# Kernel optimization log

Measured on AMD Instinct MI355X. Metric: run time of the kernel, lower is better.

The kernel has to match this reference:

```python
import jax, jax.numpy as jnp
import numpy as np

H, HEADS, LAYERS = 512, 4, 3
HD = H // HEADS
FFN = 4 * H
B, S = 4, 2048
EPS = 1e-5
SCALE_BASE = 512.0
GAMMAS = (1.0 - np.exp(np.linspace(np.log(1.0 / 32.0), np.log(1.0 / 512.0), HEADS))).astype(np.float32)


def _xpos(x, downscale):
    # x: [B, heads, L, d]; standard XPOS rotary with per-dim decay scale
    L, d = x.shape[-2], x.shape[-1]
    half = d // 2
    s = (jnp.arange(half, dtype=jnp.float32) + 0.4 * d) / (1.4 * d)          # [half]
    pos = jnp.arange(L, dtype=jnp.float32)
    scale = s[None, :] ** (pos[:, None] / SCALE_BASE)                         # [L, half]
    inv_freq = 1.0 / (10000.0 ** (jnp.arange(half, dtype=jnp.float32) / half))
    ang = pos[:, None] * inv_freq[None, :]                                    # [L, half]
    if downscale:
        scale = 1.0 / scale
    sin_s = jnp.repeat(jnp.sin(ang) * scale, 2, axis=-1)                      # [L, d]
    cos_s = jnp.repeat(jnp.cos(ang) * scale, 2, axis=-1)
    x1, x2 = x[..., 0::2], x[..., 1::2]
    rot = jnp.stack([-x2, x1], axis=-1).reshape(x.shape)                      # rotate_every_two
    return x * cos_s + rot * sin_s


def _layernorm(x, w, b):
    m = x.mean(-1, keepdims=True)
    v = ((x - m) ** 2).mean(-1, keepdims=True)
    return (x - m) / jnp.sqrt(v + EPS) * w + b


def _decay_mask(L):
    n = jnp.arange(L)
    nm = n[:, None] - n[None, :]
    g = jnp.asarray(GAMMAS)                                                   # [heads]
    # D[h,n,m] = gamma_h^(n-m) for n>=m else 0
    return jnp.where((nm >= 0)[None], g[:, None, None] ** jnp.maximum(nm, 0)[None], 0.0)


def _msr(X, WQ, WK, WV, WG, WO, gnw, gnb, D):
    # X: [B,S,H]; WQ/WK/WV: [heads,H,HD]; D: [heads,S,S]
    Q = _xpos(jnp.einsum('bsh,nhd->bnsd', X, WQ), False)
    K = _xpos(jnp.einsum('bsh,nhd->bnsd', X, WK), True)
    V = jnp.einsum('bsh,nhd->bnsd', X, WV)
    A = jnp.einsum('bnsd,bntd->bnst', Q, K) * D[None]                          # decay-weighted retention
    Y = jnp.einsum('bnst,bntd->bnsd', A, V)                                    # [B,heads,S,HD]
    Y = jnp.transpose(Y, (0, 2, 1, 3))                                         # [B,S,heads,HD] (head-major concat)
    m = Y.mean(-1, keepdims=True)
    v = ((Y - m) ** 2).mean(-1, keepdims=True)
    Yn = ((Y - m) / jnp.sqrt(v + EPS)).reshape(X.shape[0], X.shape[1], H) * gnw + gnb  # GroupNorm(heads, H)
    G = X @ WG
    return (G * jax.nn.sigmoid(G) * Yn) @ WO                                   # swish gate + out proj


def setup_inputs() -> dict:
    key = jax.random.key(0)
    ks = jax.random.split(key, 10)
    rn = lambda k, shape, sc: jax.random.normal(k, shape, jnp.float32) * sc
    return {
        'X': rn(ks[0], (B, S, H), 1.0),
        'WQ': rn(ks[1], (LAYERS, HEADS, H, HD), 1.0 / H),
        'WK': rn(ks[2], (LAYERS, HEADS, H, HD), 1.0 / H),
        'WV': rn(ks[3], (LAYERS, HEADS, H, HD), 1.0 / H),
        'WG': rn(ks[4], (LAYERS, H, H), 1.0 / H),
        'WO': rn(ks[5], (LAYERS, H, H), 1.0 / H),
        'gn_w': jnp.ones((LAYERS, H), jnp.float32),
        'gn_b': jnp.zeros((LAYERS, H), jnp.float32),
        'ln1_w': jnp.ones((LAYERS, H), jnp.float32),
        'ln1_b': jnp.zeros((LAYERS, H), jnp.float32),
        'ln2_w': jnp.ones((LAYERS, H), jnp.float32),
        'ln2_b': jnp.zeros((LAYERS, H), jnp.float32),
        'ffn_w1': rn(ks[6], (LAYERS, H, FFN), (2.0 / (H + FFN)) ** 0.5),
        'ffn_b1': jnp.zeros((LAYERS, FFN), jnp.float32),
        'ffn_w2': rn(ks[7], (LAYERS, FFN, H), (2.0 / (H + FFN)) ** 0.5),
        'ffn_b2': jnp.zeros((LAYERS, H), jnp.float32),
    }


def reference(X, WQ, WK, WV, WG, WO, gn_w, gn_b, ln1_w, ln1_b, ln2_w, ln2_b, ffn_w1, ffn_b1, ffn_w2, ffn_b2):
    D = _decay_mask(X.shape[1])
    for l in range(LAYERS):
        Y = _msr(_layernorm(X, ln1_w[l], ln1_b[l]), WQ[l], WK[l], WV[l], WG[l], WO[l], gn_w[l], gn_b[l], D) + X
        Hn = _layernorm(Y, ln2_w[l], ln2_b[l])
        X = jax.nn.gelu(Hn @ ffn_w1[l] + ffn_b1[l], approximate=False) @ ffn_w2[l] + ffn_b2[l] + Y
    return X, jnp.einsum('bsh,bth->bst', X, X)
```

## Files before the change

### kernel.cpp

```cpp
#include <hip/hip_runtime.h>
#include <math.h>

#define HH 512
#define NHEADS 4
#define HD 128
#define HALF 64
#define FFND 2048
#define BB 4
#define SS 2048
#define NLAYERS 3
#define ROWS (BB*SS)
#define EPSF 1e-5f
#define QKVGW 2048

typedef float f32x4 __attribute__((ext_vector_type(4)));
typedef float f32x16 __attribute__((ext_vector_type(16)));
typedef __bf16 bf16x8 __attribute__((ext_vector_type(8)));
typedef unsigned u32x2 __attribute__((ext_vector_type(2)));

__device__ __forceinline__ unsigned short f2bf(float f) {
    union { float f; unsigned u; } v; v.f = f;
    unsigned r = (v.u + 0x7FFFu + ((v.u >> 16) & 1u)) >> 16;
    return (unsigned short)r;
}
__device__ __forceinline__ float bf2f(unsigned short h) {
    union { unsigned u; float f; } v; v.u = ((unsigned)h) << 16;
    return v.f;
}
__device__ __forceinline__ void gl16(const void* g, void* l) {
    __builtin_amdgcn_global_load_lds((const __attribute__((address_space(1))) void*)g,
                                     (__attribute__((address_space(3))) void*)l, 16, 0, 0);
}
__device__ __forceinline__ bf16x8 ld8(const void* p) { return *(const bf16x8*)p; }
__device__ __forceinline__ unsigned laddr(void* p) {
    return (unsigned)(size_t)(__attribute__((address_space(3))) char*)p;
}
__device__ __forceinline__ u32x2 tr8(unsigned a) {
    u32x2 r;
    asm volatile("ds_read_b64_tr_b16 %0, %1" : "=v"(r) : "v"(a));
    return r;
}

__global__ void k_tables(float* __restrict__ cq, float* __restrict__ sq,
                         float* __restrict__ ck, float* __restrict__ sk) {
    int i = threadIdx.x;
    int s = blockIdx.x;
    float si   = ((float)i + 0.4f * (float)HD) / (1.4f * (float)HD);
    float scale = powf(si, (float)s / 512.0f);
    float invf = powf(10000.0f, -((float)i) / (float)HALF);
    float ang  = (float)s * invf;
    float c = cosf(ang), sn = sinf(ang);
    int idx = s * HALF + i;
    cq[idx] = c * scale;   sq[idx] = sn * scale;
    float is = 1.0f / scale;
    ck[idx] = c * is;      sk[idx] = sn * is;
}

__global__ __launch_bounds__(256) void k_wt(const float* __restrict__ src, unsigned short* __restrict__ dst,
                                            int K, int N, int zn, size_t sL, size_t sZ) {
    __shared__ float T[32][33];
    int n0 = blockIdx.x * 32, k0 = blockIdx.y * 32;
    int z = blockIdx.z;
    src += (size_t)z * (size_t)K * N;
    dst += (size_t)(z / zn) * sL + (size_t)(z % zn) * sZ;
    int tx = threadIdx.x & 31, ty = threadIdx.x >> 5;
    #pragma unroll
    for (int i = 0; i < 4; ++i) {
        int r = ty + i * 8;
        T[r][tx] = src[(size_t)(k0 + r) * N + n0 + tx];
    }
    __syncthreads();
    #pragma unroll
    for (int i = 0; i < 4; ++i) {
        int r = ty + i * 8;
        dst[(size_t)(n0 + r) * K + k0 + tx] = f2bf(T[tx][r]);
    }
}

__global__ __launch_bounds__(256) void k_ln(const float* __restrict__ x, const float* __restrict__ w,
                                            const float* __restrict__ b, unsigned short* __restrict__ y) {
    int lane = threadIdx.x & 63;
    size_t row = (size_t)blockIdx.x * 4 + (threadIdx.x >> 6);
    const float4* xr = (const float4*)(x + row * HH);
    float4 v0 = xr[lane * 2];
    float4 v1 = xr[lane * 2 + 1];
    float s  = v0.x + v0.y + v0.z + v0.w + v1.x + v1.y + v1.z + v1.w;
    float ss = v0.x*v0.x + v0.y*v0.y + v0.z*v0.z + v0.w*v0.w
             + v1.x*v1.x + v1.y*v1.y + v1.z*v1.z + v1.w*v1.w;
    for (int off = 32; off > 0; off >>= 1) {
        s  += __shfl_xor(s, off);
        ss += __shfl_xor(ss, off);
    }
    float m   = s * (1.0f / HH);
    float var = ss * (1.0f / HH) - m * m;
    float inv = rsqrtf(var + EPSF);
    int h0 = lane * 8;
    float4 wa = *(const float4*)(w + h0);
    float4 wb = *(const float4*)(w + h0 + 4);
    float4 ba = *(const float4*)(b + h0);
    float4 bb2 = *(const float4*)(b + h0 + 4);
    uint4 pk;
    pk.x = f2bf((v0.x - m) * inv * wa.x + ba.x) | ((unsigned)f2bf((v0.y - m) * inv * wa.y + ba.y) << 16);
    pk.y = f2bf((v0.z - m) * inv * wa.z + ba.z) | ((unsigned)f2bf((v0.w - m) * inv * wa.w + ba.w) << 16);
    pk.z = f2bf((v1.x - m) * inv * wb.x + bb2.x) | ((unsigned)f2bf((v1.y - m) * inv * wb.y + bb2.y) << 16);
    pk.w = f2bf((v1.z - m) * inv * wb.z + bb2.z) | ((unsigned)f2bf((v1.w - m) * inv * wb.w + bb2.w) << 16);
    *(uint4*)(y + row * HH + h0) = pk;
}

__global__ __launch_bounds__(256) void k_xpos(unsigned short* __restrict__ QG,
    const float* __restrict__ cq, const float* __restrict__ sq,
    const float* __restrict__ ck, const float* __restrict__ sk) {
    int row = blockIdx.x, p = threadIdx.x;
    int s = row & (SS - 1), n = p >> 6, i = p & 63;
    int ti = s * HALF + i;
    size_t qo = (size_t)row * QKVGW + n * HD + i * 2;
    unsigned qv = *(unsigned*)(QG + qo);
    float x1 = bf2f(qv & 0xffff), x2 = bf2f(qv >> 16);
    float c = cq[ti], sn = sq[ti];
    *(unsigned*)(QG + qo) = (unsigned)f2bf(x1 * c - x2 * sn) | ((unsigned)f2bf(x2 * c + x1 * sn) << 16);
    size_t ko = qo + 512;
    unsigned kv = *(unsigned*)(QG + ko);
    x1 = bf2f(kv & 0xffff); x2 = bf2f(kv >> 16);
    c = ck[ti]; sn = sk[ti];
    *(unsigned*)(QG + ko) = (unsigned)f2bf(x1 * c - x2 * sn) | ((unsigned)f2bf(x2 * c + x1 * sn) << 16);
}

__global__ __launch_bounds__(256) void k_zero(float* __restrict__ Y) {
    int idx = blockIdx.x * 256 + threadIdx.x;
    int bb = idx / 196608;
    int rem = idx - bb * 196608;
    float4 zz = {0.f, 0.f, 0.f, 0.f};
    *(float4*)(Y + (size_t)bb * (SS * HH) + (size_t)512 * HH + (size_t)rem * 4) = zz;
}

__global__ __launch_bounds__(256, 2) void k_ret(
    const unsigned short* __restrict__ QG, float* __restrict__ Y) {
    __shared__ __align__(16) char sm[81920];
    const int tid = threadIdx.x;
    const int lane = tid & 63, wv = tid >> 6;
    const int l31 = lane & 31, g2 = lane >> 5;
    const int b4 = (lane >> 4) & 1;
    const int bx = blockIdx.x;
    int xs, c0 = 0;
    if (bx < 16)      { xs = 15 - (bx >> 2); c0 = bx & 3; }
    else if (bx < 28) { int i = bx - 16; xs = 11 - i / 3; c0 = i % 3; }
    else if (bx < 36) { int i = bx - 28; xs = 7 - (i >> 1); c0 = i & 1; }
    else              { xs = 39 - bx; }
    const int hn = blockIdx.y, b = blockIdx.z;
    const int s0 = xs * 128;
    const int nt = 2 * xs + 2;
    const int tstart = c0 * 8;
    const int tend = min(nt, tstart + 8);
    const double la = -3.4657359027997265, lb = -6.238324625039508;
    const float gamma = (float)(1.0 - exp(la + (lb - la) * ((double)hn / 3.0)));
    const float l2g = log2f(gamma);
    const size_t rowbase = (size_t)b * SS;
    const int qcol = hn * HD, kcol = 512 + hn * HD, vcol = 1024 + hn * HD;
    const char* Gp = (const char*)QG;

    const int srow = s0 + wv * 32 + l31;
    bf16x8 qf[8];
    #pragma unroll
    for (int kc = 0; kc < 8; ++kc)
        qf[kc] = ld8(QG + (rowbase + srow) * QKVGW + qcol + kc * 16 + g2 * 8);

    float gq[4], gj[4];
    #pragma unroll
    for (int q = 0; q < 4; ++q) { gq[q] = exp2f(-l2g * (8.0f * q)); gj[q] = exp2f(-l2g * (float)q); }
    const float gt32m = exp2f(-l2g * 32.0f);

    f32x16 accy[4];
    #pragma unroll
    for (int d = 0; d < 4; ++d)
        #pragma unroll
        for (int e = 0; e < 16; ++e) accy[d][e] = 0.0f;

    const int sloc = wv * 32 + l31;
    const int ssw = (sloc & 7) << 4;
    const int r15 = (l31 & 15) << 4;

    auto stage = [&](int t0, int buf) {
        #pragma unroll
        for (int c = 0; c < 4; ++c) {
            int chunk = wv * 4 + c;
            int r = chunk * 4 + (lane >> 4);
            int w = ((lane & 15) * 16) ^ ((r & 15) << 4);
            gl16(Gp + ((rowbase + t0 + r) * QKVGW + kcol) * 2 + w, sm + buf * 16384 + chunk * 1024);
        }
        #pragma unroll
        for (int c = 0; c < 4; ++c) {
            int chunk = wv * 4 + c;
            int slot = chunk * 64 + lane;
            int sub = slot >> 3, w8 = slot & 7;
            int db = sub >> 4, tb = sub & 15;
            int tl = tb * 4 + (w8 >> 1);
            int d  = db * 16 + (w8 & 1) * 8;
            gl16(Gp + ((rowbase + t0 + tl) * QKVGW + vcol + d) * 2, sm + 32768 + buf * 16384 + chunk * 1024);
        }
    };

    int cur = 0;
    stage(tstart * 64, 0);
    for (int t = tstart; t < tend; ++t) {
        const int t0 = t * 64;
        if (t + 1 < tend) {
            stage((t + 1) * 64, cur ^ 1);
            asm volatile("s_waitcnt vmcnt(8)" ::: "memory");
        } else {
            asm volatile("s_waitcnt vmcnt(0)" ::: "memory");
        }
        __builtin_amdgcn_sched_barrier(0);
        __builtin_amdgcn_s_barrier();
        __builtin_amdgcn_sched_barrier(0);
        {
            const char* kb = sm + cur * 16384;
            f32x16 pacc0, pacc1;
            #pragma unroll
            for (int e = 0; e < 16; ++e) { pacc0[e] = 0.0f; pacc1[e] = 0.0f; }
            #pragma unroll
            for (int kc = 0; kc < 8; ++kc) {
                bf16x8 k0 = ld8(kb + l31 * 256 + ((kc * 32 + g2 * 16) ^ r15));
                bf16x8 k1 = ld8(kb + (32 + l31) * 256 + ((kc * 32 + g2 * 16) ^ r15));
                pacc0 = __builtin_amdgcn_mfma_f32_32x32x16_bf16(k0, qf[kc], pacc0, 0, 0, 0);
                pacc1 = __builtin_amdgcn_mfma_f32_32x32x16_bf16(k1, qf[kc], pacc1, 0, 0, 0);
            }
            const float G0 = exp2f(l2g * (float)(srow - t0 - g2 * 4));
            #pragma unroll
            for (int tb2 = 0; tb2 < 2; ++tb2) {
                const float gb = tb2 ? gt32m : 1.0f;
                #pragma unroll
                for (int q = 0; q < 4; ++q) {
                    int tbase = t0 + tb2 * 32 + q * 8 + g2 * 4;
                    float base = G0 * gb * gq[q];
                    float p0 = (tb2 ? pacc1 : pacc0)[q * 4 + 0];
                    float p1 = (tb2 ? pacc1 : pacc0)[q * 4 + 1];
                    float p2 = (tb2 ? pacc1 : pacc0)[q * 4 + 2];
                    float p3 = (tb2 ? pacc1 : pacc0)[q * 4 + 3];
                    unsigned short u0 = f2bf((srow >= tbase + 0) ? p0 * base * gj[0] : 0.0f);
                    unsigned short u1 = f2bf((srow >= tbase + 1) ? p1 * base * gj[1] : 0.0f);
                    unsigned short u2 = f2bf((srow >= tbase + 2) ? p2 * base * gj[2] : 0.0f);
                    unsigned short u3 = f2bf((srow >= tbase + 3) ? p3 * base * gj[3] : 0.0f);
                    u32x2 pk2;
                    pk2.x = (unsigned)u0 | ((unsigned)u1 << 16);
                    pk2.y = (unsigned)u2 | ((unsigned)u3 << 16);
                    *(u32x2*)(sm + 65536 + ((sloc * 128 + tb2 * 64 + q * 16 + g2 * 8) ^ ssw)) = pk2;
                }
            }
            bf16x8 pf[4];
            #pragma unroll
            for (int tc = 0; tc < 4; ++tc)
                pf[tc] = ld8(sm + 65536 + ((sloc * 128 + tc * 32 + g2 * 16) ^ ssw));
            const unsigned vbase = laddr(sm + 32768 + cur * 16384) + b4 * 2048 + g2 * 256 + (lane & 15) * 2;
            #pragma unroll
            for (int dblk = 0; dblk < 4; ++dblk) {
                u32x2 va[4], vb[4];
                #pragma unroll
                for (int tc = 0; tc < 4; ++tc) {
                    unsigned a0 = vbase + dblk * 4096 + tc * 512;
                    va[tc] = tr8(a0);
                    vb[tc] = tr8(a0 + 128);
                }
                asm volatile("s_waitcnt lgkmcnt(0)" ::: "memory");
                __builtin_amdgcn_sched_barrier(0);
                #pragma unroll
                for (int tc = 0; tc < 4; ++tc) {
                    union { u32x2 u[2]; bf16x8 v; } cvt;
                    cvt.u[0] = va[tc]; cvt.u[1] = vb[tc];
                    accy[dblk] = __builtin_amdgcn_mfma_f32_32x32x16_bf16(pf[tc], cvt.v, accy[dblk], 0, 0, 0);
                }
            }
        }
        __builtin_amdgcn_sched_barrier(0);
        __builtin_amdgcn_s_barrier();
        __builtin_amdgcn_sched_barrier(0);
        cur ^= 1;
    }
    if (xs < 4) {
        #pragma unroll
        for (int dblk = 0; dblk < 4; ++dblk)
            #pragma unroll
            for (int rg = 0; rg < 16; ++rg) {
                int sl2 = s0 + wv * 32 + (rg & 3) + (rg >> 2) * 8 + g2 * 4;
                Y[(rowbase + sl2) * HH + hn * HD + dblk * 32 + l31] = accy[dblk][rg];
            }
    } else {
        #pragma unroll
        for (int dblk = 0; dblk < 4; ++dblk)
            #pragma unroll
            for (int rg = 0; rg < 16; ++rg) {
                int sl2 = s0 + wv * 32 + (rg & 3) + (rg >> 2) * 8 + g2 * 4;
                unsafeAtomicAdd(&Y[(rowbase + sl2) * HH + hn * HD + dblk * 32 + l31], accy[dblk][rg]);
            }
    }
}

__global__ __launch_bounds__(256) void k_gate(
    const float* __restrict__ Yr, const unsigned short* __restrict__ QG,
    const float* __restrict__ gw, const float* __restrict__ gb,
    unsigned short* __restrict__ E) {
    int lane = threadIdx.x & 63;
    int grp  = blockIdx.x * 4 + (threadIdx.x >> 6);
    int row = grp >> 2, nh = grp & 3;
    size_t off = (size_t)row * HH + nh * HD + lane * 2;
    float2 v = *(const float2*)(Yr + off);
    float s = v.x + v.y, ss = v.x * v.x + v.y * v.y;
    for (int o = 32; o > 0; o >>= 1) {
        s  += __shfl_xor(s, o);
        ss += __shfl_xor(ss, o);
    }
    float m   = s * (1.0f / HD);
    float var = ss * (1.0f / HD) - m * m;
    float inv = rsqrtf(var + EPSF);
    int h = nh * HD + lane * 2;
    unsigned gv = *(const unsigned*)(QG + (size_t)row * QKVGW + 1536 + nh * HD + lane * 2);
    float g0 = bf2f(gv & 0xffff), g1 = bf2f(gv >> 16);
    float2 w2 = *(const float2*)(gw + h), b2 = *(const float2*)(gb + h);
    float yn0 = (v.x - m) * inv * w2.x + b2.x;
    float yn1 = (v.y - m) * inv * w2.y + b2.y;
    float e0v = g0 / (1.0f + expf(-g0)) * yn0;
    float e1v = g1 / (1.0f + expf(-g1)) * yn1;
    *(unsigned*)(E + off) = (unsigned)f2bf(e0v) | ((unsigned)f2bf(e1v) << 16);
}

template<int EPI, int OUTBF>
__global__ __launch_bounds__(256) void k_mm(
    const unsigned short* __restrict__ A, const unsigned short* __restrict__ Bt,
    void* __restrict__ Cv, const float* __restrict__ bias, const float* __restrict__ Rs,
    int M, int N, int K, size_t aB, size_t bB, size_t cB,
    unsigned short* __restrict__ C2) {
    __shared__ __align__(16) char sm[16384];
    const int tid = threadIdx.x;
    const int lane = tid & 63, wid = tid >> 6;
    const int wr = wid >> 1, wc = wid & 1;
    const int lcol = lane & 15, lrow = lane >> 4;
    const size_t m0 = (size_t)blockIdx.x * 128, n0 = (size_t)blockIdx.y * 128;
    const char* Ab = (const char*)(A + (size_t)blockIdx.z * aB);
    const char* Bb = (const char*)(Bt + (size_t)blockIdx.z * bB);
    f32x4 acc[4][4];
    #pragma unroll
    for (int i = 0; i < 4; ++i)
        #pragma unroll
        for (int j = 0; j < 4; ++j) acc[i][j] = f32x4{0.f, 0.f, 0.f, 0.f};
    for (int k0 = 0; k0 < K; k0 += 32) {
        __syncthreads();
        #pragma unroll
        for (int c = 0; c < 2; ++c) {
            int chunk = wid * 2 + c;
            int r = chunk * 16 + (lane >> 2);
            int w = ((lane & 3) ^ (r & 3)) << 4;
            gl16(Ab + ((size_t)(m0 + r) * K + k0) * 2 + w, sm + chunk * 1024);
            gl16(Bb + ((size_t)(n0 + r) * K + k0) * 2 + w, sm + 8192 + chunk * 1024);
        }
        __syncthreads();
        bf16x8 af[4], bfr[4];
        #pragma unroll
        for (int m = 0; m < 4; ++m) {
            int r = wr * 64 + m * 16 + lcol;
            af[m] = ld8(sm + r * 64 + ((lrow * 16) ^ ((r & 3) << 4)));
        }
        #pragma unroll
        for (int n2 = 0; n2 < 4; ++n2) {
            int r = wc * 64 + n2 * 16 + lcol;
            bfr[n2] = ld8(sm + 8192 + r * 64 + ((lrow * 16) ^ ((r & 3) << 4)));
        }
        #pragma unroll
        for (int m = 0; m < 4; ++m)
            #pragma unroll
            for (int n2 = 0; n2 < 4; ++n2)
                acc[m][n2] = __builtin_amdgcn_mfma_f32_16x16x32_bf16(af[m], bfr[n2], acc[m][n2], 0, 0, 0);
    }
    float* Cf = (float*)Cv + (size_t)blockIdx.z * cB;
    unsigned short* Cb = (unsigned short*)Cv + (size_t)blockIdx.z * cB;
    const float* Rb = (EPI >= 2) ? (Rs + (size_t)blockIdx.z * cB) : nullptr;
    #pragma unroll
    for (int m = 0; m < 4; ++m) {
        #pragma unroll
        for (int n2 = 0; n2 < 4; ++n2) {
            size_t col = n0 + wc * 64 + n2 * 16 + lcol;
            float bc = (EPI == 1 || EPI == 2 || EPI == 4) ? bias[col] : 0.0f;
            #pragma unroll
            for (int j = 0; j < 4; ++j) {
                size_t row = m0 + wr * 64 + m * 16 + lrow * 4 + j;
                float v = acc[m][n2][j];
                if (EPI == 1) { v += bc; v = 0.5f * v * (1.0f + erff(v * 0.70710678118654752f)); }
                else if (EPI == 2 || EPI == 4) v += bc + Rb[row * N + col];
                else if (EPI == 3) v += Rb[row * N + col];
                if (EPI == 4) {
                    Cf[row * N + col] = v;
                    C2[row * N + col] = f2bf(v);
                } else if (OUTBF) Cb[row * N + col] = f2bf(v);
                else              Cf[row * N + col] = v;
            }
        }
    }
}

extern "C" void kernel_launch(void* const* d_in, const int* in_sizes, int n_in,
                              void* d_out, int out_size, void* d_ws, size_t ws_size,
                              hipStream_t stream) {
    const float* X0  = (const float*)d_in[0];
    const float* WQ  = (const float*)d_in[1];
    const float* WK  = (const float*)d_in[2];
    const float* WV  = (const float*)d_in[3];
    const float* WG  = (const float*)d_in[4];
    const float* WO  = (const float*)d_in[5];
    const float* gnw = (const float*)d_in[6];
    const float* gnb = (const float*)d_in[7];
    const float* l1w = (const float*)d_in[8];
    const float* l1b = (const float*)d_in[9];
    const float* l2w = (const float*)d_in[10];
    const float* l2b = (const float*)d_in[11];
    const float* fw1 = (const float*)d_in[12];
    const float* fb1 = (const float*)d_in[13];
    const float* fw2 = (const float*)d_in[14];
    const float* fb2 = (const float*)d_in[15];
    float* outX = (float*)d_out;
    float* outG = outX + (size_t)ROWS * HH;

    char* wp = (char*)d_ws;
    auto take = [&](size_t bytes) { char* p = wp; wp += (bytes + 255) & ~(size_t)255; return p; };
    float* cq = (float*)take((size_t)SS * HALF * 4);
    float* sq = (float*)take((size_t)SS * HALF * 4);
    float* ck = (float*)take((size_t)SS * HALF * 4);
    float* sk = (float*)take((size_t)SS * HALF * 4);
    unsigned short* Wcat = (unsigned short*)take((size_t)NLAYERS * QKVGW * HH * 2);
    unsigned short* WOt = (unsigned short*)take((size_t)NLAYERS * HH * HH * 2);
    unsigned short* F1t = (unsigned short*)take((size_t)NLAYERS * HH * FFND * 2);
    unsigned short* F2t = (unsigned short*)take((size_t)NLAYERS * HH * FFND * 2);
    unsigned short* Xn  = (unsigned short*)take((size_t)ROWS * HH * 2);
    unsigned short* QKVG = (unsigned short*)take((size_t)ROWS * QKVGW * 2);
    unsigned short* Eb  = (unsigned short*)take((size_t)ROWS * HH * 2);
    float* Yr   = (float*)take((size_t)ROWS * HH * 4);
    float* Y2   = (float*)take((size_t)ROWS * HH * 4);
    float* Xbuf = (float*)take((size_t)ROWS * HH * 4);
    unsigned short* Hb = (unsigned short*)take((size_t)ROWS * FFND * 2);
    unsigned short* Xb = Xn;

    k_tables<<<SS, HALF, 0, stream>>>(cq, sq, ck, sk);
    k_wt<<<dim3(4, 16, 12), 256, 0, stream>>>(WQ, Wcat, HH, HD, 4, (size_t)QKVGW * HH, (size_t)HD * HH);
    k_wt<<<dim3(4, 16, 12), 256, 0, stream>>>(WK, Wcat + (size_t)512 * HH, HH, HD, 4, (size_t)QKVGW * HH, (size_t)HD * HH);
    k_wt<<<dim3(4, 16, 12), 256, 0, stream>>>(WV, Wcat + (size_t)1024 * HH, HH, HD, 4, (size_t)QKVGW * HH, (size_t)HD * HH);
    k_wt<<<dim3(16, 16, 3), 256, 0, stream>>>(WG, Wcat + (size_t)1536 * HH, HH, HH, 1, (size_t)QKVGW * HH, 0);
    k_wt<<<dim3(16, 16, 3), 256, 0, stream>>>(WO, WOt, HH, HH, 1, (size_t)HH * HH, 0);
    k_wt<<<dim3(64, 16, 3), 256, 0, stream>>>(fw1, F1t, HH, FFND, 1, (size_t)HH * FFND, 0);
    k_wt<<<dim3(16, 64, 3), 256, 0, stream>>>(fw2, F2t, FFND, HH, 1, (size_t)FFND * HH, 0);

    const float* curX = X0;
    for (int l = 0; l < NLAYERS; ++l) {
        const unsigned short* Bc = Wcat + (size_t)l * QKVGW * HH;
        const unsigned short* Bo = WOt + (size_t)l * HH * HH;
        const unsigned short* B1 = F1t + (size_t)l * HH * FFND;
        const unsigned short* B2 = F2t + (size_t)l * HH * FFND;
        k_ln<<<ROWS / 4, 256, 0, stream>>>(curX, l1w + l * HH, l1b + l * HH, Xn);
        dim3 gq(ROWS / 128, QKVGW / 128, 1);
        k_mm<0, 1><<<gq, 256, 0, stream>>>(Xn, Bc, QKVG, nullptr, nullptr, ROWS, QKVGW, HH, 0, 0, 0, nullptr);
        k_xpos<<<ROWS, 256, 0, stream>>>(QKVG, cq, sq, ck, sk);
        k_zero<<<3072, 256, 0, stream>>>(Yr);
        k_ret<<<dim3(40, NHEADS, BB), 256, 0, stream>>>(QKVG, Yr);
        k_gate<<<ROWS, 256, 0, stream>>>(Yr, QKVG, gnw + l * HH, gnb + l * HH, Eb);
        dim3 g1(ROWS / 128, HH / 128, 1);
        k_mm<3, 0><<<g1, 256, 0, stream>>>(Eb, Bo, Y2, nullptr, curX, ROWS, HH, HH, 0, 0, 0, nullptr);
        k_ln<<<ROWS / 4, 256, 0, stream>>>(Y2, l2w + l * HH, l2b + l * HH, Xn);
        dim3 g2(ROWS / 128, FFND / 128, 1);
        k_mm<1, 1><<<g2, 256, 0, stream>>>(Xn, B1, Hb, fb1 + (size_t)l * FFND, nullptr, ROWS, FFND, HH, 0, 0, 0, nullptr);
        if (l == NLAYERS - 1) {
            k_mm<4, 0><<<g1, 256, 0, stream>>>(Hb, B2, outX, fb2 + (size_t)l * HH, Y2, ROWS, HH, FFND, 0, 0, 0, Xb);
        } else {
            k_mm<2, 0><<<g1, 256, 0, stream>>>(Hb, B2, Xbuf, fb2 + (size_t)l * HH, Y2, ROWS, HH, FFND, 0, 0, 0, nullptr);
        }
        curX = Xbuf;
    }
    dim3 g3(SS / 128, SS / 128, BB);
    k_mm<0, 0><<<g3, 256, 0, stream>>>(Xb, Xb, outG, nullptr, nullptr, SS, SS, HH,
                                       (size_t)SS * HH, (size_t)SS * HH, (size_t)SS * SS, nullptr);
}
```

Before: 870.5 us.

## Replace quadratic retention with chunkwise recurrent state, scan, and intra-chunk attention

```diff
diff --git a/kernel.cpp b/kernel.cpp
--- a/kernel.cpp
+++ b/kernel.cpp
@@ -125,173 +125,270 @@
     *(unsigned*)(QG + ko) = (unsigned)f2bf(x1 * c - x2 * sn) | ((unsigned)f2bf(x2 * c + x1 * sn) << 16);
 }
 
-__global__ __launch_bounds__(256) void k_zero(float* __restrict__ Y) {
-    int idx = blockIdx.x * 256 + threadIdx.x;
-    int bb = idx / 196608;
-    int rem = idx - bb * 196608;
-    float4 zz = {0.f, 0.f, 0.f, 0.f};
-    *(float4*)(Y + (size_t)bb * (SS * HH) + (size_t)512 * HH + (size_t)rem * 4) = zz;
-}
-
-__global__ __launch_bounds__(256, 2) void k_ret(
-    const unsigned short* __restrict__ QG, float* __restrict__ Y) {
-    __shared__ __align__(16) char sm[81920];
+__global__ __launch_bounds__(256, 2) void k_state(
+    const unsigned short* __restrict__ QG, unsigned short* __restrict__ Bbuf) {
+    __shared__ __align__(16) char sm[65536];
     const int tid = threadIdx.x;
     const int lane = tid & 63, wv = tid >> 6;
     const int l31 = lane & 31, g2 = lane >> 5;
     const int b4 = (lane >> 4) & 1;
-    const int bx = blockIdx.x;
-    int xs, c0 = 0;
-    if (bx < 16)      { xs = 15 - (bx >> 2); c0 = bx & 3; }
-    else if (bx < 28) { int i = bx - 16; xs = 11 - i / 3; c0 = i % 3; }
-    else if (bx < 36) { int i = bx - 28; xs = 7 - (i >> 1); c0 = i & 1; }
-    else              { xs = 39 - bx; }
-    const int hn = blockIdx.y, b = blockIdx.z;
-    const int s0 = xs * 128;
-    const int nt = 2 * xs + 2;
-    const int tstart = c0 * 8;
-    const int tend = min(nt, tstart + 8);
+    const int c = blockIdx.x, hn = blockIdx.y, b = blockIdx.z;
+    const double la = -3.4657359027997265, lb = -6.238324625039508;
+    const float gamma = (float)(1.0 - exp(la + (lb - la) * ((double)hn / 3.0)));
+    const float l2g = log2f(gamma);
+    const size_t rowbase = (size_t)b * SS + c * 128;
+    const int kcol = 512 + hn * HD, vcol = 1024 + hn * HD;
+    const char* Gp = (const char*)QG;
+    #pragma unroll
+    for (int c2 = 0; c2 < 8; ++c2) {
+        int slot = c2 * 256 + tid;
+        int sub = slot >> 3, w8 = slot & 7;
+        int db = sub >> 5, tb = sub & 31;
+        int tl = tb * 4 + (w8 >> 1);
+        int d  = db * 16 + (w8 & 1) * 8;
+        gl16(Gp + ((rowbase + tl) * QKVGW + kcol + d) * 2, sm + slot * 16);
+        gl16(Gp + ((rowbase + tl) * QKVGW + vcol + d) * 2, sm + 32768 + slot * 16);
+    }
+    asm volatile("s_waitcnt vmcnt(0)" ::: "memory");
+    __builtin_amdgcn_s_barrier();
+    float sce[8];
+    #pragma unroll
+    for (int e = 0; e < 8; ++e) sce[e] = exp2f(l2g * (float)(128 - g2 * 8 - e));
+    f32x16 acc[4];
+    #pragma unroll
+    for (int d = 0; d < 4; ++d)
+        #pragma unroll
+        for (int e = 0; e < 16; ++e) acc[d][e] = 0.0f;
+    const unsigned kb = laddr(sm) + (wv * 2 + b4) * 4096 + g2 * 256 + (lane & 15) * 2;
+    const unsigned vb = laddr(sm + 32768) + b4 * 4096 + g2 * 256 + (lane & 15) * 2;
+    #pragma unroll
+    for (int kc = 0; kc < 8; ++kc) {
+        u32x2 ka = tr8(kb + kc * 512);
+        u32x2 kb2 = tr8(kb + kc * 512 + 128);
+        u32x2 vv[8];
+        #pragma unroll
+        for (int dblk = 0; dblk < 4; ++dblk) {
+            vv[dblk * 2]     = tr8(vb + dblk * 8192 + kc * 512);
+            vv[dblk * 2 + 1] = tr8(vb + dblk * 8192 + kc * 512 + 128);
+        }
+        asm volatile("s_waitcnt lgkmcnt(0)" ::: "memory");
+        __builtin_amdgcn_sched_barrier(0);
+        const float gkc = exp2f(l2g * (float)(-16 * kc));
+        union { u32x2 u[2]; unsigned short s[8]; bf16x8 v; } af, ap;
+        af.u[0] = ka; af.u[1] = kb2;
+        #pragma unroll
+        for (int e = 0; e < 8; ++e) ap.s[e] = f2bf(bf2f(af.s[e]) * (sce[e] * gkc));
+        #pragma unroll
+        for (int dblk = 0; dblk < 4; ++dblk) {
+            union { u32x2 u[2]; bf16x8 v; } bv;
+            bv.u[0] = vv[dblk * 2]; bv.u[1] = vv[dblk * 2 + 1];
+            acc[dblk] = __builtin_amdgcn_mfma_f32_32x32x16_bf16(ap.v, bv.v, acc[dblk], 0, 0, 0);
+        }
+    }
+    unsigned short* Bp = Bbuf + (((size_t)(b * 4 + hn) * 16 + c) * 16384);
+    #pragma unroll
+    for (int dblk = 0; dblk < 4; ++dblk)
+        #pragma unroll
+        for (int reg = 0; reg < 16; ++reg) {
+            int row = (reg & 3) + 8 * (reg >> 2) + 4 * g2 + wv * 32;
+            Bp[row * 128 + dblk * 32 + l31] = f2bf(acc[dblk][reg]);
+        }
+}
+
+__global__ __launch_bounds__(256) void k_scan(const unsigned short* __restrict__ Bbuf,
+                                              unsigned short* __restrict__ Abuf) {
+    const int tid = threadIdx.x;
+    const int rg = blockIdx.x, hn = blockIdx.y, b = blockIdx.z;
+    const double la = -3.4657359027997265, lb = -6.238324625039508;
+    const float gamma = (float)(1.0 - exp(la + (lb - la) * ((double)hn / 3.0)));
+    const float gC = exp2f(log2f(gamma) * 128.0f);
+    const size_t ubase = ((size_t)(b * 4 + hn) * 16) * 16384;
+    const size_t off = (size_t)rg * 4096 + (size_t)tid * 16;
+    float a[16];
+    #pragma unroll
+    for (int e = 0; e < 16; ++e) a[e] = 0.0f;
+    for (int c = 1; c < 16; ++c) {
+        const unsigned short* bp = Bbuf + ubase + (size_t)(c - 1) * 16384 + off;
+        uint4 u0 = *(const uint4*)bp;
+        uint4 u1 = *(const uint4*)(bp + 8);
+        const unsigned short* up0 = (const unsigned short*)&u0;
+        const unsigned short* up1 = (const unsigned short*)&u1;
+        #pragma unroll
+        for (int e = 0; e < 8; ++e) a[e] = gC * a[e] + bf2f(up0[e]);
+        #pragma unroll
+        for (int e = 0; e < 8; ++e) a[8 + e] = gC * a[8 + e] + bf2f(up1[e]);
+        uint4 o0, o1;
+        unsigned short* op0 = (unsigned short*)&o0;
+        unsigned short* op1 = (unsigned short*)&o1;
+        #pragma unroll
+        for (int e = 0; e < 8; ++e) op0[e] = f2bf(a[e]);
+        #pragma unroll
+        for (int e = 0; e < 8; ++e) op1[e] = f2bf(a[8 + e]);
+        unsigned short* ap2 = Abuf + ubase + (size_t)c * 16384 + off;
+        *(uint4*)ap2 = o0;
+        *(uint4*)(ap2 + 8) = o1;
+    }
+}
+
+__global__ __launch_bounds__(256, 1) void k_ret2(
+    const unsigned short* __restrict__ QG, const unsigned short* __restrict__ Abuf,
+    float* __restrict__ Y) {
+    __shared__ __align__(16) char sm[114688];
+    const int tid = threadIdx.x;
+    const int lane = tid & 63, wv = tid >> 6;
+    const int l31 = lane & 31, g2 = lane >> 5;
+    const int b4 = (lane >> 4) & 1;
+    const int c = blockIdx.x, hn = blockIdx.y, b = blockIdx.z;
+    const int cC = c * 128;
     const double la = -3.4657359027997265, lb = -6.238324625039508;
     const float gamma = (float)(1.0 - exp(la + (lb - la) * ((double)hn / 3.0)));
     const float l2g = log2f(gamma);
     const size_t rowbase = (size_t)b * SS;
     const int qcol = hn * HD, kcol = 512 + hn * HD, vcol = 1024 + hn * HD;
     const char* Gp = (const char*)QG;
-
-    const int srow = s0 + wv * 32 + l31;
+    const int srow = cC + wv * 32 + l31;
     bf16x8 qf[8];
     #pragma unroll
     for (int kc = 0; kc < 8; ++kc)
         qf[kc] = ld8(QG + (rowbase + srow) * QKVGW + qcol + kc * 16 + g2 * 8);
-
-    float gq[4], gj[4];
-    #pragma unroll
-    for (int q = 0; q < 4; ++q) { gq[q] = exp2f(-l2g * (8.0f * q)); gj[q] = exp2f(-l2g * (float)q); }
-    const float gt32m = exp2f(-l2g * 32.0f);
-
+    #pragma unroll
+    for (int cc = 0; cc < 4; ++cc) {
+        int chunk = wv * 4 + cc;
+        int r = chunk * 4 + (lane >> 4);
+        int w = ((lane & 15) * 16) ^ ((r & 15) << 4);
+        gl16(Gp + ((rowbase + cC + r) * QKVGW + kcol) * 2 + w, sm + chunk * 1024);
+        gl16(Gp + ((rowbase + cC + 64 + r) * QKVGW + kcol) * 2 + w, sm + 16384 + chunk * 1024);
+        int slot = chunk * 64 + lane;
+        int sub = slot >> 3, w8 = slot & 7;
+        int db = sub >> 4, tb = sub & 15;
+        int tl = tb * 4 + (w8 >> 1);
+        int d  = db * 16 + (w8 & 1) * 8;
+        gl16(Gp + ((rowbase + cC + tl) * QKVGW + vcol + d) * 2, sm + 32768 + slot * 16);
+        gl16(Gp + ((rowbase + cC + 64 + tl) * QKVGW + vcol + d) * 2, sm + 49152 + slot * 16);
+    }
+    if (c > 0) {
+        const char* Ap = (const char*)(Abuf + (((size_t)(b * 4 + hn) * 16 + c) * 16384));
+        #pragma unroll
+        for (int c2 = 0; c2 < 8; ++c2) {
+            int slot = c2 * 256 + tid;
+            int sub = slot >> 3, w8 = slot & 7;
+            int db = sub >> 5, tb = sub & 31;
+            int row = tb * 4 + (w8 >> 1);
+            int d   = db * 16 + (w8 & 1) * 8;
+            gl16(Ap + (row * 128 + d) * 2, sm + 65536 + slot * 16);
+        }
+    }
+    asm volatile("s_waitcnt vmcnt(0)" ::: "memory");
+    __builtin_amdgcn_s_barrier();
     f32x16 accy[4];
     #pragma unroll
     for (int d = 0; d < 4; ++d)
         #pragma unroll
         for (int e = 0; e < 16; ++e) accy[d][e] = 0.0f;
-
-    const int sloc = wv * 32 + l31;
-    const int ssw = (sloc & 7) << 4;
-    const int r15 = (l31 & 15) << 4;
-
-    auto stage = [&](int t0, int buf) {
-        #pragma unroll
-        for (int c = 0; c < 4; ++c) {
-            int chunk = wv * 4 + c;
-            int r = chunk * 4 + (lane >> 4);
-            int w = ((lane & 15) * 16) ^ ((r & 15) << 4);
-            gl16(Gp + ((rowbase + t0 + r) * QKVGW + kcol) * 2 + w, sm + buf * 16384 + chunk * 1024);
-        }
-        #pragma unroll
-        for (int c = 0; c < 4; ++c) {
-            int chunk = wv * 4 + c;
-            int slot = chunk * 64 + lane;
-            int sub = slot >> 3, w8 = slot & 7;
-            int db = sub >> 4, tb = sub & 15;
-            int tl = tb * 4 + (w8 >> 1);
-            int d  = db * 16 + (w8 & 1) * 8;
-            gl16(Gp + ((rowbase + t0 + tl) * QKVGW + vcol + d) * 2, sm + 32768 + buf * 16384 + chunk * 1024);
-        }
-    };
-
-    int cur = 0;
-    stage(tstart * 64, 0);
-    for (int t = tstart; t < tend; ++t) {
-        const int t0 = t * 64;
-        if (t + 1 < tend) {
-            stage((t + 1) * 64, cur ^ 1);
-            asm volatile("s_waitcnt vmcnt(8)" ::: "memory");
-        } else {
-            asm volatile("s_waitcnt vmcnt(0)" ::: "memory");
-        }
-        __builtin_amdgcn_sched_barrier(0);
-        __builtin_amdgcn_s_barrier();
-        __builtin_amdgcn_sched_barrier(0);
-        {
-            const char* kb = sm + cur * 16384;
-            f32x16 pacc0, pacc1;
-            #pragma unroll
-            for (int e = 0; e < 16; ++e) { pacc0[e] = 0.0f; pacc1[e] = 0.0f; }
-            #pragma unroll
-            for (int kc = 0; kc < 8; ++kc) {
-                bf16x8 k0 = ld8(kb + l31 * 256 + ((kc * 32 + g2 * 16) ^ r15));
-                bf16x8 k1 = ld8(kb + (32 + l31) * 256 + ((kc * 32 + g2 * 16) ^ r15));
-                pacc0 = __builtin_amdgcn_mfma_f32_32x32x16_bf16(k0, qf[kc], pacc0, 0, 0, 0);
-                pacc1 = __builtin_amdgcn_mfma_f32_32x32x16_bf16(k1, qf[kc], pacc1, 0, 0, 0);
-            }
-            const float G0 = exp2f(l2g * (float)(srow - t0 - g2 * 4));
-            #pragma unroll
-            for (int tb2 = 0; tb2 < 2; ++tb2) {
-                const float gb = tb2 ? gt32m : 1.0f;
+    if (c > 0) {
+        const unsigned ab = laddr(sm + 65536) + b4 * 4096 + g2 * 256 + (lane & 15) * 2;
+        #pragma unroll
+        for (int dblk = 0; dblk < 4; ++dblk) {
+            #pragma unroll
+            for (int h = 0; h < 2; ++h) {
+                u32x2 av[8];
                 #pragma unroll
-                for (int q = 0; q < 4; ++q) {
-                    int tbase = t0 + tb2 * 32 + q * 8 + g2 * 4;
-                    float base = G0 * gb * gq[q];
-                    float p0 = (tb2 ? pacc1 : pacc0)[q * 4 + 0];
-                    float p1 = (tb2 ? pacc1 : pacc0)[q * 4 + 1];
-                    float p2 = (tb2 ? pacc1 : pacc0)[q * 4 + 2];
-                    float p3 = (tb2 ? pacc1 : pacc0)[q * 4 + 3];
-                    unsigned short u0 = f2bf((srow >= tbase + 0) ? p0 * base * gj[0] : 0.0f);
-                    unsigned short u1 = f2bf((srow >= tbase + 1) ? p1 * base * gj[1] : 0.0f);
-                    unsigned short u2 = f2bf((srow >= tbase + 2) ? p2 * base * gj[2] : 0.0f);
-                    unsigned short u3 = f2bf((srow >= tbase + 3) ? p3 * base * gj[3] : 0.0f);
-                    u32x2 pk2;
-                    pk2.x = (unsigned)u0 | ((unsigned)u1 << 16);
-                    pk2.y = (unsigned)u2 | ((unsigned)u3 << 16);
-                    *(u32x2*)(sm + 65536 + ((sloc * 128 + tb2 * 64 + q * 16 + g2 * 8) ^ ssw)) = pk2;
-                }
-            }
-            bf16x8 pf[4];
-            #pragma unroll
-            for (int tc = 0; tc < 4; ++tc)
-                pf[tc] = ld8(sm + 65536 + ((sloc * 128 + tc * 32 + g2 * 16) ^ ssw));
-            const unsigned vbase = laddr(sm + 32768 + cur * 16384) + b4 * 2048 + g2 * 256 + (lane & 15) * 2;
-            #pragma unroll
-            for (int dblk = 0; dblk < 4; ++dblk) {
-                u32x2 va[4], vb[4];
-                #pragma unroll
-                for (int tc = 0; tc < 4; ++tc) {
-                    unsigned a0 = vbase + dblk * 4096 + tc * 512;
-                    va[tc] = tr8(a0);
-                    vb[tc] = tr8(a0 + 128);
+                for (int kc = 0; kc < 4; ++kc) {
+                    unsigned a0 = ab + dblk * 8192 + (h * 4 + kc) * 512;
+                    av[kc * 2] = tr8(a0);
+                    av[kc * 2 + 1] = tr8(a0 + 128);
                 }
                 asm volatile("s_waitcnt lgkmcnt(0)" ::: "memory");
                 __builtin_amdgcn_sched_barrier(0);
                 #pragma unroll
-                for (int tc = 0; tc < 4; ++tc) {
-                    union { u32x2 u[2]; bf16x8 v; } cvt;
-                    cvt.u[0] = va[tc]; cvt.u[1] = vb[tc];
-                    accy[dblk] = __builtin_amdgcn_mfma_f32_32x32x16_bf16(pf[tc], cvt.v, accy[dblk], 0, 0, 0);
+                for (int kc = 0; kc < 4; ++kc) {
+                    union { u32x2 u[2]; bf16x8 v; } bv;
+                    bv.u[0] = av[kc * 2]; bv.u[1] = av[kc * 2 + 1];
+                    accy[dblk] = __builtin_amdgcn_mfma_f32_32x32x16_bf16(qf[h * 4 + kc], bv.v, accy[dblk], 0, 0, 0);
                 }
             }
         }
-        __builtin_amdgcn_sched_barrier(0);
-        __builtin_amdgcn_s_barrier();
-        __builtin_amdgcn_sched_barrier(0);
-        cur ^= 1;
-    }
-    if (xs < 4) {
-        #pragma unroll
-        for (int dblk = 0; dblk < 4; ++dblk)
-            #pragma unroll
-            for (int rg = 0; rg < 16; ++rg) {
-                int sl2 = s0 + wv * 32 + (rg & 3) + (rg >> 2) * 8 + g2 * 4;
-                Y[(rowbase + sl2) * HH + hn * HD + dblk * 32 + l31] = accy[dblk][rg];
+        #pragma unroll
+        for (int reg = 0; reg < 16; ++reg) {
+            float gsc = exp2f(l2g * (float)(wv * 32 + (reg & 3) + 8 * (reg >> 2) + 4 * g2));
+            #pragma unroll
+            for (int dblk = 0; dblk < 4; ++dblk) accy[dblk][reg] *= gsc;
+        }
+    }
+    const int sloc = wv * 32 + l31;
+    const int ssw = (sloc & 7) << 4;
+    const int r15 = (l31 & 15) << 4;
+    float gq[4], gj[4];
+    #pragma unroll
+    for (int q = 0; q < 4; ++q) { gq[q] = exp2f(-l2g * (8.0f * q)); gj[q] = exp2f(-l2g * (float)q); }
+    const float gt32m = exp2f(-l2g * 32.0f);
+    const int ntt = (wv >> 1) + 1;
+    for (int tt = 0; tt < ntt; ++tt) {
+        const int t0 = cC + tt * 64;
+        const char* kb = sm + tt * 16384;
+        f32x16 pacc0, pacc1;
+        #pragma unroll
+        for (int e = 0; e < 16; ++e) { pacc0[e] = 0.0f; pacc1[e] = 0.0f; }
+        #pragma unroll
+        for (int kc = 0; kc < 8; ++kc) {
+            bf16x8 k0 = ld8(kb + l31 * 256 + ((kc * 32 + g2 * 16) ^ r15));
+            bf16x8 k1 = ld8(kb + (32 + l31) * 256 + ((kc * 32 + g2 * 16) ^ r15));
+            pacc0 = __builtin_amdgcn_mfma_f32_32x32x16_bf16(k0, qf[kc], pacc0, 0, 0, 0);
+            pacc1 = __builtin_amdgcn_mfma_f32_32x32x16_bf16(k1, qf[kc], pacc1, 0, 0, 0);
+        }
+        const float G0 = exp2f(l2g * (float)(srow - t0 - g2 * 4));
+        #pragma unroll
+        for (int tb2 = 0; tb2 < 2; ++tb2) {
+            const float gb = tb2 ? gt32m : 1.0f;
+            #pragma unroll
+            for (int q = 0; q < 4; ++q) {
+                int tbase = t0 + tb2 * 32 + q * 8 + g2 * 4;
+                float base = G0 * gb * gq[q];
+                float p0 = (tb2 ? pacc1 : pacc0)[q * 4 + 0];
+                float p1 = (tb2 ? pacc1 : pacc0)[q * 4 + 1];
+                float p2 = (tb2 ? pacc1 : pacc0)[q * 4 + 2];
+                float p3 = (tb2 ? pacc1 : pacc0)[q * 4 + 3];
+                unsigned short u0 = f2bf((srow >= tbase + 0) ? p0 * base * gj[0] : 0.0f);
+                unsigned short u1 = f2bf((srow >= tbase + 1) ? p1 * base * gj[1] : 0.0f);
+                unsigned short u2 = f2bf((srow >= tbase + 2) ? p2 * base * gj[2] : 0.0f);
+                unsigned short u3 = f2bf((srow >= tbase + 3) ? p3 * base * gj[3] : 0.0f);
+                u32x2 pk2;
+                pk2.x = (unsigned)u0 | ((unsigned)u1 << 16);
+                pk2.y = (unsigned)u2 | ((unsigned)u3 << 16);
+                *(u32x2*)(sm + 98304 + ((sloc * 128 + tb2 * 64 + q * 16 + g2 * 8) ^ ssw)) = pk2;
             }
-    } else {
-        #pragma unroll
-        for (int dblk = 0; dblk < 4; ++dblk)
-            #pragma unroll
-            for (int rg = 0; rg < 16; ++rg) {
-                int sl2 = s0 + wv * 32 + (rg & 3) + (rg >> 2) * 8 + g2 * 4;
-                unsafeAtomicAdd(&Y[(rowbase + sl2) * HH + hn * HD + dblk * 32 + l31], accy[dblk][rg]);
+        }
+        bf16x8 pf[4];
+        #pragma unroll
+        for (int tc = 0; tc < 4; ++tc)
+            pf[tc] = ld8(sm + 98304 + ((sloc * 128 + tc * 32 + g2 * 16) ^ ssw));
+        const unsigned vbase = laddr(sm + 32768 + tt * 16384) + b4 * 2048 + g2 * 256 + (lane & 15) * 2;
+        #pragma unroll
+        for (int dblk = 0; dblk < 4; ++dblk) {
+            u32x2 va[4], vb2[4];
+            #pragma unroll
+            for (int tc = 0; tc < 4; ++tc) {
+                unsigned a0 = vbase + dblk * 4096 + tc * 512;
+                va[tc] = tr8(a0);
+                vb2[tc] = tr8(a0 + 128);
             }
-    }
+            asm volatile("s_waitcnt lgkmcnt(0)" ::: "memory");
+            __builtin_amdgcn_sched_barrier(0);
+            #pragma unroll
+            for (int tc = 0; tc < 4; ++tc) {
+                union { u32x2 u[2]; bf16x8 v; } cvt;
+                cvt.u[0] = va[tc]; cvt.u[1] = vb2[tc];
+                accy[dblk] = __builtin_amdgcn_mfma_f32_32x32x16_bf16(pf[tc], cvt.v, accy[dblk], 0, 0, 0);
+            }
+        }
+    }
+    #pragma unroll
+    for (int dblk = 0; dblk < 4; ++dblk)
+        #pragma unroll
+        for (int rg = 0; rg < 16; ++rg) {
+            int sl2 = cC + wv * 32 + (rg & 3) + (rg >> 2) * 8 + g2 * 4;
+            Y[(rowbase + sl2) * HH + hn * HD + dblk * 32 + l31] = accy[dblk][rg];
+        }
 }
 
 __global__ __launch_bounds__(256) void k_gate(
@@ -435,6 +532,8 @@
     float* Xbuf = (float*)take((size_t)ROWS * HH * 4);
     unsigned short* Hb = (unsigned short*)take((size_t)ROWS * FFND * 2);
     unsigned short* Xb = Xn;
+    unsigned short* Bbuf = (unsigned short*)Y2;
+    unsigned short* Abuf = Bbuf + (size_t)4194304;
 
     k_tables<<<SS, HALF, 0, stream>>>(cq, sq, ck, sk);
     k_wt<<<dim3(4, 16, 12), 256, 0, stream>>>(WQ, Wcat, HH, HD, 4, (size_t)QKVGW * HH, (size_t)HD * HH);
@@ -455,8 +554,9 @@
         dim3 gq(ROWS / 128, QKVGW / 128, 1);
         k_mm<0, 1><<<gq, 256, 0, stream>>>(Xn, Bc, QKVG, nullptr, nullptr, ROWS, QKVGW, HH, 0, 0, 0, nullptr);
         k_xpos<<<ROWS, 256, 0, stream>>>(QKVG, cq, sq, ck, sk);
-        k_zero<<<3072, 256, 0, stream>>>(Yr);
-        k_ret<<<dim3(40, NHEADS, BB), 256, 0, stream>>>(QKVG, Yr);
+        k_state<<<dim3(16, NHEADS, BB), 256, 0, stream>>>(QKVG, Bbuf);
+        k_scan<<<dim3(4, NHEADS, BB), 256, 0, stream>>>(Bbuf, Abuf);
+        k_ret2<<<dim3(16, NHEADS, BB), 256, 0, stream>>>(QKVG, Abuf, Yr);
         k_gate<<<ROWS, 256, 0, stream>>>(Yr, QKVG, gnw + l * HH, gnb + l * HH, Eb);
         dim3 g1(ROWS / 128, HH / 128, 1);
         k_mm<3, 0><<<g1, 256, 0, stream>>>(Eb, Bo, Y2, nullptr, curX, ROWS, HH, HH, 0, 0, 0, nullptr);
```

New measurement: 917.5 us. 5.4% more time.
